# Optimization experiments

Hardware: AMD Instinct MI355X
Metric: run time of the kernel (lower is better)

Reference implementation:

```python
import jax, jax.numpy as jnp
import numpy as np

E = 256
H = 8
B = 131072
N_ATTN = 6  # gd, gc, dg, dc, cg, cd


def setup_inputs() -> dict:
    key = jax.random.key(0)
    ks = jax.random.split(key, 16)
    s = 0.05  # init scale ~ 1/sqrt(E)
    inp = {
        "genomic_embed": jax.random.normal(ks[0], (B, E), jnp.float32),
        "drug_embed": jax.random.normal(ks[1], (B, E), jnp.float32),
        "clinical_embed": jax.random.normal(ks[2], (B, E), jnp.float32),
        # six MultiheadAttention modules, stacked along axis 0
        "Wq": jax.random.normal(ks[3], (N_ATTN, E, E), jnp.float32) * s,
        "Wk": jax.random.normal(ks[4], (N_ATTN, E, E), jnp.float32) * s,
        "Wv": jax.random.normal(ks[5], (N_ATTN, E, E), jnp.float32) * s,
        "bq": jax.random.normal(ks[6], (N_ATTN, E), jnp.float32) * s,
        "bk": jax.random.normal(ks[7], (N_ATTN, E), jnp.float32) * s,
        "bv": jax.random.normal(ks[8], (N_ATTN, E), jnp.float32) * s,
        "Wo": jax.random.normal(ks[9], (N_ATTN, E, E), jnp.float32) * s,
        "bo": jax.random.normal(ks[10], (N_ATTN, E), jnp.float32) * s,
        # fusion MLP: Linear(3E -> 2E), ReLU, Linear(2E -> E)
        "W1": jax.random.normal(ks[11], (2 * E, 3 * E), jnp.float32) * s,
        "b1": jax.random.normal(ks[12], (2 * E,), jnp.float32) * s,
        "W2": jax.random.normal(ks[13], (E, 2 * E), jnp.float32) * s,
        "b2": jax.random.normal(ks[14], (E,), jnp.float32) * s,
    }
    return inp


def _mha1(q_in, kv_in, Wq, Wk, Wv, bq, bk, bv, Wo, bo):
    """MultiheadAttention with seq_len=1 for both query and key/value.
    q_in, kv_in: [B, E]. Returns [B, E]. Dropout is eval-mode identity."""
    D = E // H
    q = (q_in @ Wq.T + bq).reshape(-1, H, D)
    k = (kv_in @ Wk.T + bk).reshape(-1, H, D)
    v = (kv_in @ Wv.T + bv).reshape(-1, H, D)
    # single key: scores [B, H, 1]; softmax over the 1-key axis is identically 1,
    # kept for mathematical faithfulness to the original module
    scores = jnp.sum(q * k, axis=-1, keepdims=True) / jnp.sqrt(jnp.float32(D))
    attn = jax.nn.softmax(scores, axis=-1)
    out = (attn * v).reshape(-1, E)
    return out @ Wo.T + bo


def reference(genomic_embed, drug_embed, clinical_embed,
              Wq, Wk, Wv, bq, bk, bv, Wo, bo, W1, b1, W2, b2):
    g, d, c = genomic_embed, drug_embed, clinical_embed
    # six cross attentions: (query, kv) pairs in module order
    def att(i, q_in, kv_in):
        return _mha1(q_in, kv_in, Wq[i], Wk[i], Wv[i],
                     bq[i], bk[i], bv[i], Wo[i], bo[i])
    gd = att(0, g, d)
    gc = att(1, g, c)
    dg = att(2, d, g)
    dc = att(3, d, c)
    cg = att(4, c, g)
    cd = att(5, c, d)
    g_att = g + gd + gc
    d_att = d + dg + dc
    c_att = c + cg + cd
    combined = jnp.concatenate([g_att, d_att, c_att], axis=-1)  # [B, 3E]
    hidden = jax.nn.relu(combined @ W1.T + b1)                  # [B, 2E]
    fused = hidden @ W2.T + b2                                  # [B, E]
    return fused
```

## Files before the change

kernel.cpp:

```cpp
#include <hip/hip_runtime.h>
#include <cstdint>
#include <cstddef>


typedef __attribute__((ext_vector_type(8))) short short8;
typedef __attribute__((ext_vector_type(4))) float float4v;

__device__ __forceinline__ unsigned short f2bf(float f) {
  union { float f; unsigned u; } v; v.f = f;
  unsigned r = v.u + 0x7FFFu + ((v.u >> 16) & 1u);
  return (unsigned short)(r >> 16);
}

__global__ __launch_bounds__(256) void k_prep1(const float* __restrict__ Wo,
                                               const float* __restrict__ Wv,
                                               const float* __restrict__ bv,
                                               const float* __restrict__ bo,
                                               float* __restrict__ Wf,
                                               float* __restrict__ bfs) {
  __shared__ float red[256];
  int b = blockIdx.x;
  if (b < 1536) {
    int i = b >> 8, m = b & 255;
    int n = threadIdx.x;
    const float* wo = Wo + i * 65536 + m * 256;
    const float* wv = Wv + i * 65536 + n;
    float a0 = 0.f, a1 = 0.f, a2 = 0.f, a3 = 0.f;
#pragma unroll 4
    for (int k = 0; k < 256; k += 4) {
      a0 += wo[k]     * wv[k * 256];
      a1 += wo[k + 1] * wv[(k + 1) * 256];
      a2 += wo[k + 2] * wv[(k + 2) * 256];
      a3 += wo[k + 3] * wv[(k + 3) * 256];
    }
    Wf[i * 65536 + m * 256 + n] = (a0 + a1) + (a2 + a3);
  } else {
    int bb = b - 1536;
    int p = bb >> 8, m = bb & 255;
    int t = threadIdx.x;
    int a = 2 * p, b2i = 2 * p + 1;
    float v = Wo[a * 65536 + m * 256 + t] * bv[a * 256 + t]
            + Wo[b2i * 65536 + m * 256 + t] * bv[b2i * 256 + t];
    red[t] = v; __syncthreads();
    for (int s = 128; s > 0; s >>= 1) { if (t < s) red[t] += red[t + s]; __syncthreads(); }
    if (t == 0) bfs[p * 256 + m] = red[0] + bo[a * 256 + m] + bo[b2i * 256 + m];
  }
}

__global__ __launch_bounds__(256) void k_prep2(const float* __restrict__ W1,
                                               const float* __restrict__ b1,
                                               const float* __restrict__ Wf,
                                               const float* __restrict__ bfs,
                                               const float* __restrict__ W2,
                                               unsigned short* __restrict__ ATS,
                                               float* __restrict__ bias_h,
                                               unsigned short* __restrict__ W2p) {
  __shared__ float red[256];
  int b = blockIdx.x;
  if (b < 1536) {
    int n = b & 511, p = b >> 9;
    int kk = threadIdx.x;
    int fA, oA, fB, oB;
    if (p == 0)      { fA = 2; oA = 256; fB = 4; oB = 512; }
    else if (p == 1) { fA = 0; oA = 0;   fB = 5; oB = 512; }
    else             { fA = 1; oA = 0;   fB = 3; oB = 256; }
    const float* w1n = W1 + n * 768;
    const float* wfa = Wf + fA * 65536 + kk;
    const float* wfb = Wf + fB * 65536 + kk;
    float v0 = w1n[p * 256 + kk], v1 = 0.f, v2 = 0.f, v3 = 0.f;
#pragma unroll 4
    for (int j = 0; j < 256; j += 2) {
      v0 += w1n[oA + j]     * wfa[j * 256];
      v1 += w1n[oA + j + 1] * wfa[(j + 1) * 256];
      v2 += w1n[oB + j]     * wfb[j * 256];
      v3 += w1n[oB + j + 1] * wfb[(j + 1) * 256];
    }
    float val = (v0 + v1) + (v2 + v3);
    int k = p * 256 + kk;
    int t = k >> 5, kq = (k >> 3) & 3, j8 = k & 7;
    int unit = n * 4 + (kq ^ (n & 3));
    ATS[t * 16384 + unit * 8 + j8] = f2bf(val);
  } else if (b < 2048) {
    int n = b - 1536;
    int kk = threadIdx.x;
    const float* w1n = W1 + n * 768;
    float v = w1n[kk] * bfs[kk] + w1n[256 + kk] * bfs[256 + kk] +
              w1n[512 + kk] * bfs[512 + kk];
    red[kk] = v; __syncthreads();
    for (int s = 128; s > 0; s >>= 1) { if (kk < s) red[kk] += red[kk + s]; __syncthreads(); }
    if (kk == 0) bias_h[n] = red[0] + b1[n];
  } else {
    int id = (b - 2048) * 256 + threadIdx.x;
    int cpos = id >> 14;
    int n = (id >> 6) & 255;
    int kp = id & 63;
    int t = kp >> 4, ci = kp & 15;
    W2p[id] = f2bf(W2[n * 512 + (cpos + 8 * t) * 16 + ci]);
  }
}

__global__ __launch_bounds__(512, 2) void k_main(
    const float* __restrict__ G, const float* __restrict__ D,
    const float* __restrict__ C, const unsigned short* __restrict__ ATS,
    const float* __restrict__ bias_h, const unsigned short* __restrict__ W2p,
    const float* __restrict__ b2, float* __restrict__ Out) {
  __shared__ unsigned short ats[2][16384];
  __shared__ unsigned short xt[128][40];
  __shared__ unsigned short hid[128][72];

  const int tid = threadIdx.x;
  const int lane = tid & 63, wave = tid >> 6;
  const int l15 = lane & 15, lq = lane >> 4;
  const int m0 = blockIdx.x * 128;
  const int wm = wave >> 2, wn = wave & 3;

  float4v acc1[4][8];
#pragma unroll
  for (int j = 0; j < 8; ++j) {
    float bh = bias_h[wn * 128 + j * 16 + l15];
#pragma unroll
    for (int i = 0; i < 4; ++i) acc1[i][j] = (float4v){bh, bh, bh, bh};
  }

  const int xrow = tid >> 2, xseg = tid & 3;
  const int xoff = (m0 + xrow) * 256 + xseg * 8;

  float4v f0, f1, g0, g1;

#define ISSUE_X(kt1, ra, rb) do {                                           \
    int kt_ = (kt1);                                                        \
    const float* xb_ = (kt_ < 8) ? G : (kt_ < 16) ? D : C;                  \
    const float* xp_ = xb_ + xoff + (kt_ & 7) * 32;                         \
    ra = *(const float4v*)xp_;                                              \
    rb = *(const float4v*)(xp_ + 4);                                        \
  } while (0)

#define ISSUE_A(kt1, buf) do {                                              \
    const char* gsrc_ = (const char*)ATS + (size_t)(kt1) * 32768;           \
    char* ldst_ = (char*)&ats[buf][0];                                      \
    _Pragma("unroll")                                                       \
    for (int it_ = 0; it_ < 4; ++it_)                                       \
      __builtin_amdgcn_global_load_lds(                                     \
          (const __attribute__((address_space(1))) unsigned int*)(gsrc_ + it_ * 8192 + tid * 16), \
          (__attribute__((address_space(3))) unsigned int*)(ldst_ + it_ * 8192 + tid * 16), \
          16, 0, 0);                                                        \
  } while (0)

#define BODY(kt_, buf, fa, fb, ga, gb, PREF) do {                           \
    if (PREF) { ISSUE_X((kt_) + 1, ga, gb); ISSUE_A((kt_) + 1, (buf) ^ 1); } \
    short8 xv_;                                                             \
    xv_[0] = f2bf(fa[0]); xv_[1] = f2bf(fa[1]);                             \
    xv_[2] = f2bf(fa[2]); xv_[3] = f2bf(fa[3]);                             \
    xv_[4] = f2bf(fb[0]); xv_[5] = f2bf(fb[1]);                             \
    xv_[6] = f2bf(fb[2]); xv_[7] = f2bf(fb[3]);                             \
    *(short8*)&xt[xrow][xseg * 8] = xv_;                                    \
    if (PREF) asm volatile("s_waitcnt vmcnt(6) lgkmcnt(0)" ::: "memory");   \
    else      asm volatile("s_waitcnt vmcnt(0) lgkmcnt(0)" ::: "memory");   \
    __builtin_amdgcn_s_barrier();                                           \
    __builtin_amdgcn_sched_barrier(0);                                      \
    short8 a_[4];                                                           \
    _Pragma("unroll")                                                       \
    for (int i_ = 0; i_ < 4; ++i_)                                          \
      a_[i_] = *(const short8*)&xt[wm * 64 + i_ * 16 + l15][lq * 8];        \
    _Pragma("unroll")                                                       \
    for (int j_ = 0; j_ < 8; ++j_) {                                        \
      int n_ = wn * 128 + j_ * 16 + l15;                                    \
      int unit_ = n_ * 4 + (lq ^ (n_ & 3));                                 \
      short8 bf_ = *(const short8*)&ats[buf][unit_ * 8];                    \
      _Pragma("unroll")                                                     \
      for (int i_ = 0; i_ < 4; ++i_)                                        \
        acc1[i_][j_] = __builtin_amdgcn_mfma_f32_16x16x32_bf16(a_[i_], bf_, acc1[i_][j_], 0, 0, 0); \
    }                                                                       \
    __builtin_amdgcn_sched_barrier(0);                                      \
    __builtin_amdgcn_s_barrier();                                           \
  } while (0)

  ISSUE_X(0, f0, f1);
  ISSUE_A(0, 0);

  for (int kp = 0; kp < 11; ++kp) {
    BODY(2 * kp,     0, f0, f1, g0, g1, 1);
    BODY(2 * kp + 1, 1, g0, g1, f0, f1, 1);
  }
  BODY(22, 0, f0, f1, g0, g1, 1);
  BODY(23, 1, g0, g1, f0, f1, 0);

#undef BODY
#undef ISSUE_A
#undef ISSUE_X

  const int om = wave >> 2, on = wave & 3;
  float4v acc2[4][4];
#pragma unroll
  for (int j = 0; j < 4; ++j) {
    float bb = b2[on * 64 + j * 16 + l15];
#pragma unroll
    for (int i = 0; i < 4; ++i) acc2[i][j] = (float4v){bb, bb, bb, bb};
  }

#pragma unroll
  for (int cpos = 0; cpos < 8; ++cpos) {
#pragma unroll
    for (int i = 0; i < 4; ++i) {
#pragma unroll
      for (int r = 0; r < 4; ++r) {
        float v = acc1[i][cpos][r];
        v = v > 0.f ? v : 0.f;
        hid[wm * 64 + i * 16 + lq * 4 + r][wn * 16 + l15] = f2bf(v);
      }
    }
    asm volatile("s_waitcnt lgkmcnt(0)" ::: "memory");
    __builtin_amdgcn_s_barrier();
    __builtin_amdgcn_sched_barrier(0);
#pragma unroll
    for (int ks = 0; ks < 2; ++ks) {
      short8 a2[4];
#pragma unroll
      for (int i = 0; i < 4; ++i)
        a2[i] = *(const short8*)&hid[om * 64 + i * 16 + l15][ks * 32 + lq * 8];
#pragma unroll
      for (int j = 0; j < 4; ++j) {
        int n = on * 64 + j * 16 + l15;
        const unsigned short* bp = W2p + ((size_t)(cpos * 256 + n) * 64 + ks * 32 + lq * 8);
        short8 bfrag = *(const short8*)bp;
#pragma unroll
        for (int i = 0; i < 4; ++i)
          acc2[i][j] = __builtin_amdgcn_mfma_f32_16x16x32_bf16(a2[i], bfrag, acc2[i][j], 0, 0, 0);
      }
    }
    __builtin_amdgcn_sched_barrier(0);
    __builtin_amdgcn_s_barrier();
  }

#pragma unroll
  for (int i = 0; i < 4; ++i) {
#pragma unroll
    for (int r = 0; r < 4; ++r) {
      int row = m0 + om * 64 + i * 16 + lq * 4 + r;
      float* op = Out + (size_t)row * 256 + on * 64 + l15;
#pragma unroll
      for (int j = 0; j < 4; ++j) op[j * 16] = acc2[i][j][r];
    }
  }
}

extern "C" void kernel_launch(void* const* d_in, const int* in_sizes, int n_in,
                              void* d_out, int out_size, void* d_ws, size_t ws_size,
                              hipStream_t stream) {
  const float* G  = (const float*)d_in[0];
  const float* D  = (const float*)d_in[1];
  const float* C  = (const float*)d_in[2];
  const float* Wv = (const float*)d_in[5];
  const float* bv = (const float*)d_in[8];
  const float* Wo = (const float*)d_in[9];
  const float* bo = (const float*)d_in[10];
  const float* W1 = (const float*)d_in[11];
  const float* b1 = (const float*)d_in[12];
  const float* W2 = (const float*)d_in[13];
  const float* b2 = (const float*)d_in[14];

  char* ws = (char*)d_ws;
  float* Wf           = (float*)(ws);
  float* bfs          = (float*)(ws + 1572864);
  float* bias_h       = (float*)(ws + 1575936);
  unsigned short* ATS = (unsigned short*)(ws + 1577984);
  unsigned short* W2p = (unsigned short*)(ws + 2364416);
  float* Out = (float*)d_out;

  hipLaunchKernelGGL(k_prep1, dim3(2304), dim3(256), 0, stream, Wo, Wv, bv, bo, Wf, bfs);
  hipLaunchKernelGGL(k_prep2, dim3(2560), dim3(256), 0, stream, W1, b1, Wf, bfs, W2, ATS, bias_h, W2p);
  hipLaunchKernelGGL(k_main,  dim3(1024), dim3(512), 0, stream, G, D, C, ATS, bias_h, W2p, b2, Out);
}
```

Measured before the change: 584.2 us.

## Use 1024-thread blocks with triple-buffered A tiles and chunked second GEMM

The main kernel moves from 512 to 1024 threads per block (16 waves, one block per CU). Each wave now owns a 64-column slice of the hidden layer, and a third LDS buffer gives a two-stage-ahead prefetch of the weight tiles and inputs. The second GEMM is restructured so each hidden chunk is written by a single wave group into a double-buffered LDS tile, while all waves consume the previous chunk. W2 is repacked so B-fragment loads are contiguous, the LDS swizzle is changed, and k_prep1 is vectorised with float4 loads. The trade-off is lower occupancy and more barriers in the second stage, in exchange for less per-wave register pressure and deeper load overlap.

Result: no change. 593.9 us (+1.7%).

```diff
diff --git a/kernel.cpp b/kernel.cpp
--- a/kernel.cpp
+++ b/kernel.cpp
@@ -4,6 +4,7 @@
 
 
 typedef __attribute__((ext_vector_type(8))) short short8;
+typedef __attribute__((ext_vector_type(4))) short short4v;
 typedef __attribute__((ext_vector_type(4))) float float4v;
 
 __device__ __forceinline__ unsigned short f2bf(float f) {
@@ -20,22 +21,22 @@
                                                float* __restrict__ bfs) {
   __shared__ float red[256];
   int b = blockIdx.x;
-  if (b < 1536) {
-    int i = b >> 8, m = b & 255;
-    int n = threadIdx.x;
-    const float* wo = Wo + i * 65536 + m * 256;
-    const float* wv = Wv + i * 65536 + n;
-    float a0 = 0.f, a1 = 0.f, a2 = 0.f, a3 = 0.f;
-#pragma unroll 4
-    for (int k = 0; k < 256; k += 4) {
-      a0 += wo[k]     * wv[k * 256];
-      a1 += wo[k + 1] * wv[(k + 1) * 256];
-      a2 += wo[k + 2] * wv[(k + 2) * 256];
-      a3 += wo[k + 3] * wv[(k + 3) * 256];
-    }
-    Wf[i * 65536 + m * 256 + n] = (a0 + a1) + (a2 + a3);
+  if (b < 384) {
+    int i = b >> 6, mq = b & 63;
+    int mr = threadIdx.x >> 6, nv = threadIdx.x & 63;
+    const float* wo = Wo + i * 65536 + (mq * 4 + mr) * 256;
+    const float* wv = Wv + i * 65536 + nv * 4;
+    float4v a0 = {0.f, 0.f, 0.f, 0.f}, a1 = {0.f, 0.f, 0.f, 0.f};
+#pragma unroll 8
+    for (int k = 0; k < 256; k += 2) {
+      float4v v0 = *(const float4v*)(wv + (size_t)k * 256);
+      float4v v1 = *(const float4v*)(wv + (size_t)(k + 1) * 256);
+      a0 += wo[k] * v0;
+      a1 += wo[k + 1] * v1;
+    }
+    *(float4v*)(Wf + i * 65536 + (mq * 4 + mr) * 256 + nv * 4) = a0 + a1;
   } else {
-    int bb = b - 1536;
+    int bb = b - 384;
     int p = bb >> 8, m = bb & 255;
     int t = threadIdx.x;
     int a = 2 * p, b2i = 2 * p + 1;
@@ -78,7 +79,7 @@
     float val = (v0 + v1) + (v2 + v3);
     int k = p * 256 + kk;
     int t = k >> 5, kq = (k >> 3) & 3, j8 = k & 7;
-    int unit = n * 4 + (kq ^ (n & 3));
+    int unit = n * 4 + (kq ^ ((n >> 1) & 3));
     ATS[t * 16384 + unit * 8 + j8] = f2bf(val);
   } else if (b < 2048) {
     int n = b - 1536;
@@ -91,152 +92,164 @@
     if (kk == 0) bias_h[n] = red[0] + b1[n];
   } else {
     int id = (b - 2048) * 256 + threadIdx.x;
-    int cpos = id >> 14;
-    int n = (id >> 6) & 255;
-    int kp = id & 63;
-    int t = kp >> 4, ci = kp & 15;
-    W2p[id] = f2bf(W2[n * 512 + (cpos + 8 * t) * 16 + ci]);
-  }
-}
-
-__global__ __launch_bounds__(512, 2) void k_main(
+    int e  = id & 7;
+    int n  = (id >> 3) & 255;
+    int lq = (id >> 11) & 3;
+    int ks = (id >> 13) & 1;
+    int c  = id >> 14;
+    W2p[id] = f2bf(W2[n * 512 + c * 64 + ks * 32 + lq * 8 + e]);
+  }
+}
+
+__global__ __launch_bounds__(1024, 1) void k_main(
     const float* __restrict__ G, const float* __restrict__ D,
     const float* __restrict__ C, const unsigned short* __restrict__ ATS,
     const float* __restrict__ bias_h, const unsigned short* __restrict__ W2p,
     const float* __restrict__ b2, float* __restrict__ Out) {
-  __shared__ unsigned short ats[2][16384];
-  __shared__ unsigned short xt[128][40];
-  __shared__ unsigned short hid[128][72];
+  __shared__ unsigned short ats[3][16384];
+  __shared__ unsigned short hid[2][128][72];
+
+  unsigned short (*xt)[72] = hid[0];
 
   const int tid = threadIdx.x;
   const int lane = tid & 63, wave = tid >> 6;
   const int l15 = lane & 15, lq = lane >> 4;
   const int m0 = blockIdx.x * 128;
-  const int wm = wave >> 2, wn = wave & 3;
-
-  float4v acc1[4][8];
-#pragma unroll
-  for (int j = 0; j < 8; ++j) {
-    float bh = bias_h[wn * 128 + j * 16 + l15];
+  const int wm = wave >> 3, wn = wave & 7;
+
+  float4v acc1[4][4];
+#pragma unroll
+  for (int j = 0; j < 4; ++j) {
+    float bh = bias_h[wn * 64 + j * 16 + l15];
 #pragma unroll
     for (int i = 0; i < 4; ++i) acc1[i][j] = (float4v){bh, bh, bh, bh};
   }
 
-  const int xrow = tid >> 2, xseg = tid & 3;
-  const int xoff = (m0 + xrow) * 256 + xseg * 8;
-
-  float4v f0, f1, g0, g1;
-
-#define ISSUE_X(kt1, ra, rb) do {                                           \
+  const int xrow = tid >> 3, xseg = tid & 7;
+  const int xoff = (m0 + xrow) * 256 + xseg * 4;
+
+  float4v xs0, xs1, xs2;
+
+#define ISSUE_X(kt1, dst) do {                                              \
     int kt_ = (kt1);                                                        \
     const float* xb_ = (kt_ < 8) ? G : (kt_ < 16) ? D : C;                  \
-    const float* xp_ = xb_ + xoff + (kt_ & 7) * 32;                         \
-    ra = *(const float4v*)xp_;                                              \
-    rb = *(const float4v*)(xp_ + 4);                                        \
+    dst = *(const float4v*)(xb_ + xoff + (kt_ & 7) * 32);                   \
   } while (0)
 
 #define ISSUE_A(kt1, buf) do {                                              \
     const char* gsrc_ = (const char*)ATS + (size_t)(kt1) * 32768;           \
     char* ldst_ = (char*)&ats[buf][0];                                      \
-    _Pragma("unroll")                                                       \
-    for (int it_ = 0; it_ < 4; ++it_)                                       \
-      __builtin_amdgcn_global_load_lds(                                     \
-          (const __attribute__((address_space(1))) unsigned int*)(gsrc_ + it_ * 8192 + tid * 16), \
-          (__attribute__((address_space(3))) unsigned int*)(ldst_ + it_ * 8192 + tid * 16), \
-          16, 0, 0);                                                        \
-  } while (0)
-
-#define BODY(kt_, buf, fa, fb, ga, gb, PREF) do {                           \
-    if (PREF) { ISSUE_X((kt_) + 1, ga, gb); ISSUE_A((kt_) + 1, (buf) ^ 1); } \
-    short8 xv_;                                                             \
-    xv_[0] = f2bf(fa[0]); xv_[1] = f2bf(fa[1]);                             \
-    xv_[2] = f2bf(fa[2]); xv_[3] = f2bf(fa[3]);                             \
-    xv_[4] = f2bf(fb[0]); xv_[5] = f2bf(fb[1]);                             \
-    xv_[6] = f2bf(fb[2]); xv_[7] = f2bf(fb[3]);                             \
-    *(short8*)&xt[xrow][xseg * 8] = xv_;                                    \
-    if (PREF) asm volatile("s_waitcnt vmcnt(6) lgkmcnt(0)" ::: "memory");   \
-    else      asm volatile("s_waitcnt vmcnt(0) lgkmcnt(0)" ::: "memory");   \
+    __builtin_amdgcn_global_load_lds(                                       \
+        (const __attribute__((address_space(1))) unsigned int*)(gsrc_ + tid * 16), \
+        (__attribute__((address_space(3))) unsigned int*)(ldst_ + tid * 16), \
+        16, 0, 0);                                                          \
+    __builtin_amdgcn_global_load_lds(                                       \
+        (const __attribute__((address_space(1))) unsigned int*)(gsrc_ + 16384 + tid * 16), \
+        (__attribute__((address_space(3))) unsigned int*)(ldst_ + 16384 + tid * 16), \
+        16, 0, 0);                                                          \
+  } while (0)
+
+#define BODY(kt_, buf_, XCUR, XFUT, PREF, WAITS) do {                       \
+    if (PREF) { ISSUE_A((kt_) + 2, ((buf_) + 2) % 3); ISSUE_X((kt_) + 2, XFUT); } \
+    {                                                                       \
+      short4v xv_;                                                          \
+      xv_[0] = f2bf(XCUR[0]); xv_[1] = f2bf(XCUR[1]);                       \
+      xv_[2] = f2bf(XCUR[2]); xv_[3] = f2bf(XCUR[3]);                       \
+      *(short4v*)&xt[xrow][xseg * 4] = xv_;                                 \
+    }                                                                       \
+    asm volatile("s_waitcnt vmcnt(" WAITS ") lgkmcnt(0)" ::: "memory");     \
     __builtin_amdgcn_s_barrier();                                           \
     __builtin_amdgcn_sched_barrier(0);                                      \
-    short8 a_[4];                                                           \
-    _Pragma("unroll")                                                       \
-    for (int i_ = 0; i_ < 4; ++i_)                                          \
-      a_[i_] = *(const short8*)&xt[wm * 64 + i_ * 16 + l15][lq * 8];        \
-    _Pragma("unroll")                                                       \
-    for (int j_ = 0; j_ < 8; ++j_) {                                        \
-      int n_ = wn * 128 + j_ * 16 + l15;                                    \
-      int unit_ = n_ * 4 + (lq ^ (n_ & 3));                                 \
-      short8 bf_ = *(const short8*)&ats[buf][unit_ * 8];                    \
+    {                                                                       \
+      short8 a_[4];                                                         \
       _Pragma("unroll")                                                     \
       for (int i_ = 0; i_ < 4; ++i_)                                        \
-        acc1[i_][j_] = __builtin_amdgcn_mfma_f32_16x16x32_bf16(a_[i_], bf_, acc1[i_][j_], 0, 0, 0); \
+        a_[i_] = *(const short8*)&xt[wm * 64 + i_ * 16 + l15][lq * 8];      \
+      _Pragma("unroll")                                                     \
+      for (int j_ = 0; j_ < 4; ++j_) {                                      \
+        int n_ = wn * 64 + j_ * 16 + l15;                                   \
+        int unit_ = n_ * 4 + (lq ^ ((n_ >> 1) & 3));                        \
+        short8 bf_ = *(const short8*)&ats[buf_][unit_ * 8];                 \
+        _Pragma("unroll")                                                   \
+        for (int i_ = 0; i_ < 4; ++i_)                                      \
+          acc1[i_][j_] = __builtin_amdgcn_mfma_f32_16x16x32_bf16(a_[i_], bf_, acc1[i_][j_], 0, 0, 0); \
+      }                                                                     \
     }                                                                       \
     __builtin_amdgcn_sched_barrier(0);                                      \
     __builtin_amdgcn_s_barrier();                                           \
   } while (0)
 
-  ISSUE_X(0, f0, f1);
-  ISSUE_A(0, 0);
-
-  for (int kp = 0; kp < 11; ++kp) {
-    BODY(2 * kp,     0, f0, f1, g0, g1, 1);
-    BODY(2 * kp + 1, 1, g0, g1, f0, f1, 1);
-  }
-  BODY(22, 0, f0, f1, g0, g1, 1);
-  BODY(23, 1, g0, g1, f0, f1, 0);
+  ISSUE_A(0, 0); ISSUE_X(0, xs0);
+  ISSUE_A(1, 1); ISSUE_X(1, xs1);
+
+  for (int kp = 0; kp < 7; ++kp) {
+    BODY(3 * kp,     0, xs0, xs2, 1, "6");
+    BODY(3 * kp + 1, 1, xs1, xs0, 1, "6");
+    BODY(3 * kp + 2, 2, xs2, xs1, 1, "6");
+  }
+  BODY(21, 0, xs0, xs2, 1, "6");
+  BODY(22, 1, xs1, xs0, 0, "3");
+  BODY(23, 2, xs2, xs1, 0, "0");
 
 #undef BODY
 #undef ISSUE_A
 #undef ISSUE_X
 
   const int om = wave >> 2, on = wave & 3;
-  float4v acc2[4][4];
+  float4v acc2[2][4];
 #pragma unroll
   for (int j = 0; j < 4; ++j) {
     float bb = b2[on * 64 + j * 16 + l15];
-#pragma unroll
-    for (int i = 0; i < 4; ++i) acc2[i][j] = (float4v){bb, bb, bb, bb};
-  }
-
-#pragma unroll
-  for (int cpos = 0; cpos < 8; ++cpos) {
-#pragma unroll
-    for (int i = 0; i < 4; ++i) {
-#pragma unroll
-      for (int r = 0; r < 4; ++r) {
-        float v = acc1[i][cpos][r];
-        v = v > 0.f ? v : 0.f;
-        hid[wm * 64 + i * 16 + lq * 4 + r][wn * 16 + l15] = f2bf(v);
+    acc2[0][j] = (float4v){bb, bb, bb, bb};
+    acc2[1][j] = (float4v){bb, bb, bb, bb};
+  }
+
+#define WRITE_CHUNK(cw) do {                                                \
+    _Pragma("unroll")                                                       \
+    for (int i_ = 0; i_ < 4; ++i_)                                          \
+      _Pragma("unroll")                                                     \
+      for (int j_ = 0; j_ < 4; ++j_)                                        \
+        _Pragma("unroll")                                                   \
+        for (int r_ = 0; r_ < 4; ++r_) {                                    \
+          float v_ = acc1[i_][j_][r_];                                      \
+          v_ = v_ > 0.f ? v_ : 0.f;                                         \
+          hid[(cw) & 1][wm * 64 + i_ * 16 + lq * 4 + r_][j_ * 16 + l15] = f2bf(v_); \
+        }                                                                   \
+  } while (0)
+
+  if (wn == 0) WRITE_CHUNK(0);
+  asm volatile("s_waitcnt lgkmcnt(0)" ::: "memory");
+  __builtin_amdgcn_s_barrier();
+
+  for (int c = 0; c < 8; ++c) {
+    if (c < 7 && wn == c + 1) WRITE_CHUNK(c + 1);
+    const unsigned short (*hb)[72] = hid[c & 1];
+#pragma unroll
+    for (int ks = 0; ks < 2; ++ks) {
+      short8 a2_[2];
+#pragma unroll
+      for (int i = 0; i < 2; ++i)
+        a2_[i] = *(const short8*)&hb[om * 32 + i * 16 + l15][ks * 32 + lq * 8];
+#pragma unroll
+      for (int j = 0; j < 4; ++j) {
+        int n = on * 64 + j * 16 + l15;
+        const unsigned short* bp = W2p + ((size_t)(((c * 2 + ks) * 4 + lq) * 256 + n) * 8);
+        short8 bfrag = *(const short8*)bp;
+#pragma unroll
+        for (int i = 0; i < 2; ++i)
+          acc2[i][j] = __builtin_amdgcn_mfma_f32_16x16x32_bf16(a2_[i], bfrag, acc2[i][j], 0, 0, 0);
       }
     }
     asm volatile("s_waitcnt lgkmcnt(0)" ::: "memory");
     __builtin_amdgcn_s_barrier();
-    __builtin_amdgcn_sched_barrier(0);
-#pragma unroll
-    for (int ks = 0; ks < 2; ++ks) {
-      short8 a2[4];
-#pragma unroll
-      for (int i = 0; i < 4; ++i)
-        a2[i] = *(const short8*)&hid[om * 64 + i * 16 + l15][ks * 32 + lq * 8];
-#pragma unroll
-      for (int j = 0; j < 4; ++j) {
-        int n = on * 64 + j * 16 + l15;
-        const unsigned short* bp = W2p + ((size_t)(cpos * 256 + n) * 64 + ks * 32 + lq * 8);
-        short8 bfrag = *(const short8*)bp;
-#pragma unroll
-        for (int i = 0; i < 4; ++i)
-          acc2[i][j] = __builtin_amdgcn_mfma_f32_16x16x32_bf16(a2[i], bfrag, acc2[i][j], 0, 0, 0);
-      }
-    }
-    __builtin_amdgcn_sched_barrier(0);
-    __builtin_amdgcn_s_barrier();
-  }
-
-#pragma unroll
-  for (int i = 0; i < 4; ++i) {
+  }
+#undef WRITE_CHUNK
+
+#pragma unroll
+  for (int i = 0; i < 2; ++i) {
 #pragma unroll
     for (int r = 0; r < 4; ++r) {
-      int row = m0 + om * 64 + i * 16 + lq * 4 + r;
+      int row = m0 + om * 32 + i * 16 + lq * 4 + r;
       float* op = Out + (size_t)row * 256 + on * 64 + l15;
 #pragma unroll
       for (int j = 0; j < 4; ++j) op[j * 16] = acc2[i][j][r];
@@ -267,7 +280,7 @@
   unsigned short* W2p = (unsigned short*)(ws + 2364416);
   float* Out = (float*)d_out;
 
-  hipLaunchKernelGGL(k_prep1, dim3(2304), dim3(256), 0, stream, Wo, Wv, bv, bo, Wf, bfs);
+  hipLaunchKernelGGL(k_prep1, dim3(1152), dim3(256), 0, stream, Wo, Wv, bv, bo, Wf, bfs);
   hipLaunchKernelGGL(k_prep2, dim3(2560), dim3(256), 0, stream, W1, b1, Wf, bfs, W2, ATS, bias_h, W2p);
-  hipLaunchKernelGGL(k_main,  dim3(1024), dim3(512), 0, stream, G, D, C, ATS, bias_h, W2p, b2, Out);
-}
+  hipLaunchKernelGGL(k_main,  dim3(1024), dim3(1024), 0, stream, G, D, C, ATS, bias_h, W2p, b2, Out);
+}
```
